# Performance work log

Hardware: AMD Instinct MI355X
Metric: run time of the kernel (lower is better)

The kernel has to match this reference:

```python
import jax, jax.numpy as jnp
import numpy as np

ROT_DIM = 32  # min(32, dim_head)

def rotate_half(t):
    # '... (j d) -> ... j d' with j=2, unbind, cat(-x2, x1)
    x1, x2 = jnp.split(t, 2, axis=-1)
    return jnp.concatenate((-x2, x1), axis=-1)

def apply_rotary(pos, t):
    rot_dim = pos.shape[-1]
    t_rot, t_pass = t[..., :rot_dim], t[..., rot_dim:]
    t_rot = t_rot * jnp.cos(pos) + rotate_half(t_rot) * jnp.sin(pos)
    return jnp.concatenate((t_rot, t_pass), axis=-1)

def setup_inputs() -> dict:
    key = jax.random.key(0)
    k1, k2, k3 = jax.random.split(key, 3)
    b, n, dim = 2, 2048, 2048
    inner = 16 * 128
    x = jax.random.normal(k1, (b, n, dim), dtype=jnp.float32)
    w_qkv = jax.random.normal(k2, (3 * inner, dim), dtype=jnp.float32) * (dim ** -0.5)
    w_out = jax.random.normal(k3, (inner, dim), dtype=jnp.float32) * (inner ** -0.5)
    g = jnp.ones((dim,), dtype=jnp.float32)
    return {"x": x, "w_qkv": w_qkv, "w_out": w_out, "g": g}

def reference(x, w_qkv, w_out, g):
    b, n, dim = x.shape
    h, d = 16, 128
    scale = d ** -0.5
    # NOTE: original code computes qkv from RAW x; the LayerNorm result is unused.
    qkv = jnp.einsum('bnc,fc->bnf', x, w_qkv)  # [b, n, 3*h*d]
    q, k, v = jnp.split(qkv, 3, axis=-1)
    def to_heads(t):  # b n (h d) -> (b h) n d
        return t.reshape(b, n, h, d).transpose(0, 2, 1, 3).reshape(b * h, n, d)
    q, k, v = map(to_heads, (q, k, v))
    # rotary positions: freqs [n, ROT_DIM//2], cat -> [n, ROT_DIM]
    inv_freq = 1.0 / (10000.0 ** (jnp.arange(0, ROT_DIM, 2, dtype=jnp.float32) / ROT_DIM))
    freqs = jnp.arange(n, dtype=jnp.float32)[:, None] * inv_freq[None, :]
    pos = jnp.concatenate((freqs, freqs), axis=-1)  # [n, ROT_DIM]
    q = apply_rotary(pos, q)
    k = apply_rotary(pos, k)
    q = q * scale
    sim = jnp.einsum('bid,bjd->bij', q, k)  # [(b h), n, n]
    causal_mask = jnp.triu(jnp.ones((n, n), dtype=bool), 1)
    neg = -jnp.finfo(sim.dtype).max
    sim = jnp.where(causal_mask[None], neg, sim)
    attn = jax.nn.softmax(sim, axis=-1)
    out = jnp.einsum('bij,bjd->bid', attn, v)  # [(b h), n, d]
    out = out.reshape(b, h, n, d).transpose(0, 2, 1, 3).reshape(b, n, h * d)
    return jnp.einsum('bnf,fc->bnc', out, w_out.T)  # Linear(inner, dim): y = out @ w_out^T with w_out [inner, dim]? see note
```

## Files before the change

### kernel.cpp

```cpp
#include <hip/hip_runtime.h>
#include <hip/hip_bf16.h>
#include <stdint.h>

typedef __bf16 bf16_t;
typedef __bf16 bf16x8 __attribute__((ext_vector_type(8)));
typedef float  f32x4  __attribute__((ext_vector_type(4)));

__device__ __forceinline__ void gload16(const void* gp, void* lp) {
  __builtin_amdgcn_global_load_lds(
      (const __attribute__((address_space(1))) void*)(uintptr_t)gp,
      (__attribute__((address_space(3))) void*)(uintptr_t)lp,
      16, 0, 0);
}

__device__ __forceinline__ f32x4 mfma16(bf16x8 a, bf16x8 b, f32x4 c) {
  return __builtin_amdgcn_mfma_f32_16x16x32_bf16(a, b, c, 0, 0, 0);
}

__device__ __forceinline__ uint32_t pack2(float a, float b) {
  uint16_t ba = __builtin_bit_cast(uint16_t, (bf16_t)a);
  uint16_t bb = __builtin_bit_cast(uint16_t, (bf16_t)b);
  return (uint32_t)ba | ((uint32_t)bb << 16);
}

__global__ __launch_bounds__(256) void cast_f32_to_bf16(const float* __restrict__ in,
                                                        bf16_t* __restrict__ out, int n8) {
  int i = blockIdx.x * 256 + threadIdx.x;
  int stride = gridDim.x * 256;
  for (; i < n8; i += stride) {
    const f32x4* p = (const f32x4*)in + (size_t)i * 2;
    f32x4 a = p[0], b = p[1];
    bf16x8 o;
    o[0] = (bf16_t)a[0]; o[1] = (bf16_t)a[1]; o[2] = (bf16_t)a[2]; o[3] = (bf16_t)a[3];
    o[4] = (bf16_t)b[0]; o[5] = (bf16_t)b[1]; o[6] = (bf16_t)b[2]; o[7] = (bf16_t)b[3];
    ((bf16x8*)out)[i] = o;
  }
}

__global__ __launch_bounds__(512, 2) void gemm_qkv(const bf16_t* __restrict__ A,
                                                   const bf16_t* __restrict__ B,
                                                   bf16_t* __restrict__ C,
                                                   int M, int N, int K) {
  __shared__ __align__(16) bf16_t As[2][256 * 32];
  __shared__ __align__(16) bf16_t Bs[2][384 * 32];
  const int t = threadIdx.x;
  const int wid = t >> 6, l = t & 63;
  const int l15 = l & 15, l4 = l >> 4;
  const int wm = wid >> 2, wn = wid & 3;
  const long m0 = (long)blockIdx.x * 256;
  const long n0 = (long)blockIdx.y * 384;
  const int KT = K >> 5;

  auto stageA = [&](int kt, bf16_t* __restrict__ LB) {
    #pragma unroll
    for (int it = 0; it < 2; ++it) {
      int s = it * 512 + t;
      int r = s >> 2, c = s & 3;
      gload16(A + (m0 + r) * (long)K + kt * 32 + c * 8, LB + r * 32 + c * 8);
    }
  };
  auto stageB = [&](int kt, bf16_t* __restrict__ LB) {
    #pragma unroll
    for (int it = 0; it < 3; ++it) {
      int s = it * 512 + t;
      int r = s >> 2, c = s & 3;
      gload16(B + (n0 + r) * (long)K + kt * 32 + c * 8, LB + r * 32 + c * 8);
    }
  };
  auto ldfrag = [&](const bf16_t* buf, int rloc) -> bf16x8 {
    return *(const bf16x8*)(buf + rloc * 32 + l4 * 8);
  };

  f32x4 acc[8][6] = {};

  stageB(0, &Bs[0][0]);
  stageA(0, &As[0][0]);
  stageB(1, &Bs[1][0]);
  asm volatile("s_waitcnt vmcnt(3)" ::: "memory");
  asm volatile("s_barrier" ::: "memory");

  for (int kt = 0; kt < KT; ++kt) {
    const bf16_t* Ab = &As[kt & 1][0];
    const bf16_t* Bb = &Bs[kt & 1][0];
    const bool stA = (kt + 1 < KT), stB = (kt + 2 < KT);

    bf16x8 bfr[6];
    #pragma unroll
    for (int nr = 0; nr < 6; ++nr) bfr[nr] = ldfrag(Bb, wn * 96 + nr * 16 + l15);
    {
      bf16x8 a0 = ldfrag(Ab, wm * 128 + 0 * 16 + l15);
      bf16x8 a1 = ldfrag(Ab, wm * 128 + 1 * 16 + l15);
      bf16x8 a2 = ldfrag(Ab, wm * 128 + 2 * 16 + l15);
      bf16x8 a3 = ldfrag(Ab, wm * 128 + 3 * 16 + l15);
      if (stA) stageA(kt + 1, &As[(kt + 1) & 1][0]);
      asm volatile("s_barrier" ::: "memory");
      asm volatile("s_waitcnt lgkmcnt(0)" ::: "memory");
      __builtin_amdgcn_sched_barrier(0);
      __builtin_amdgcn_s_setprio(1);
      #pragma unroll
      for (int nr = 0; nr < 6; ++nr) {
        acc[0][nr] = mfma16(a0, bfr[nr], acc[0][nr]);
        acc[1][nr] = mfma16(a1, bfr[nr], acc[1][nr]);
        acc[2][nr] = mfma16(a2, bfr[nr], acc[2][nr]);
        acc[3][nr] = mfma16(a3, bfr[nr], acc[3][nr]);
      }
      __builtin_amdgcn_s_setprio(0);
      asm volatile("s_barrier" ::: "memory");
    }
    {
      bf16x8 a4 = ldfrag(Ab, wm * 128 + 4 * 16 + l15);
      bf16x8 a5 = ldfrag(Ab, wm * 128 + 5 * 16 + l15);
      bf16x8 a6 = ldfrag(Ab, wm * 128 + 6 * 16 + l15);
      bf16x8 a7 = ldfrag(Ab, wm * 128 + 7 * 16 + l15);
      if (stB) stageB(kt + 2, &Bs[kt & 1][0]);
      asm volatile("s_barrier" ::: "memory");
      asm volatile("s_waitcnt lgkmcnt(0)" ::: "memory");
      __builtin_amdgcn_sched_barrier(0);
      __builtin_amdgcn_s_setprio(1);
      #pragma unroll
      for (int nr = 0; nr < 6; ++nr) {
        acc[4][nr] = mfma16(a4, bfr[nr], acc[4][nr]);
        acc[5][nr] = mfma16(a5, bfr[nr], acc[5][nr]);
        acc[6][nr] = mfma16(a6, bfr[nr], acc[6][nr]);
        acc[7][nr] = mfma16(a7, bfr[nr], acc[7][nr]);
      }
      __builtin_amdgcn_s_setprio(0);
      if (stB) asm volatile("s_waitcnt vmcnt(3)" ::: "memory");
      else     asm volatile("s_waitcnt vmcnt(0)" ::: "memory");
      asm volatile("s_barrier" ::: "memory");
    }
  }

  #pragma unroll
  for (int mr = 0; mr < 8; ++mr)
    #pragma unroll
    for (int nr = 0; nr < 6; ++nr)
      #pragma unroll
      for (int i = 0; i < 4; ++i) {
        long r = m0 + wm * 128 + mr * 16 + l4 * 4 + i;
        long c = n0 + wn * 96 + nr * 16 + l15;
        C[r * N + c] = (bf16_t)acc[mr][nr][i];
      }
}

template<bool OUT_BF16>
__global__ __launch_bounds__(512, 2) void gemm8p_bt(const bf16_t* __restrict__ A,
                                                    const bf16_t* __restrict__ B,
                                                    void* __restrict__ Cout,
                                                    int M, int N, int K) {
  __shared__ __align__(16) bf16_t As[2][128 * 64];
  __shared__ __align__(16) bf16_t Bs[2][256 * 64];
  const int t = threadIdx.x;
  const int wid = t >> 6, l = t & 63;
  const int l15 = l & 15, l4 = l >> 4;
  const int wm = wid >> 2, wn = wid & 3;
  const long m0 = (long)blockIdx.x * 128;
  const long n0 = (long)blockIdx.y * 256;
  const int KT = K >> 6;

  auto stageA = [&](int kt, bf16_t* __restrict__ LB) {
    #pragma unroll
    for (int it = 0; it < 2; ++it) {
      int s = it * 512 + t;
      int r = s >> 3, c = s & 7;
      gload16(A + (m0 + r) * (long)K + kt * 64 + ((c ^ (r & 7)) << 3),
              LB + r * 64 + c * 8);
    }
  };
  auto stageB = [&](int kt, bf16_t* __restrict__ LB) {
    #pragma unroll
    for (int it = 0; it < 4; ++it) {
      int s = it * 512 + t;
      int r = s >> 3, c = s & 7;
      gload16(B + (n0 + r) * (long)K + kt * 64 + ((c ^ (r & 7)) << 3),
              LB + r * 64 + c * 8);
    }
  };
  auto ldfrag = [&](const bf16_t* buf, int rloc, int kk) -> bf16x8 {
    return *(const bf16x8*)(buf + rloc * 64 + ((((kk << 2) + l4) ^ (rloc & 7)) << 3));
  };

  f32x4 acc[4][4] = {};

  stageB(0, &Bs[0][0]);
  stageA(0, &As[0][0]);
  stageB(1, &Bs[1][0]);
  asm volatile("s_waitcnt vmcnt(4)" ::: "memory");
  asm volatile("s_barrier" ::: "memory");

  for (int kt = 0; kt < KT; ++kt) {
    const bf16_t* Ab = &As[kt & 1][0];
    const bf16_t* Bb = &Bs[kt & 1][0];
    const bool stA = (kt + 1 < KT), stB = (kt + 2 < KT);

    bf16x8 bfr[4][2];
    #pragma unroll
    for (int nr = 0; nr < 4; ++nr)
      #pragma unroll
      for (int kk = 0; kk < 2; ++kk)
        bfr[nr][kk] = ldfrag(Bb, wn * 64 + nr * 16 + l15, kk);
    {
      bf16x8 a00 = ldfrag(Ab, wm * 64 + 0 * 16 + l15, 0);
      bf16x8 a01 = ldfrag(Ab, wm * 64 + 0 * 16 + l15, 1);
      bf16x8 a10 = ldfrag(Ab, wm * 64 + 1 * 16 + l15, 0);
      bf16x8 a11 = ldfrag(Ab, wm * 64 + 1 * 16 + l15, 1);
      if (stA) stageA(kt + 1, &As[(kt + 1) & 1][0]);
      asm volatile("s_barrier" ::: "memory");
      asm volatile("s_waitcnt lgkmcnt(0)" ::: "memory");
      __builtin_amdgcn_sched_barrier(0);
      __builtin_amdgcn_s_setprio(1);
      #pragma unroll
      for (int nr = 0; nr < 4; ++nr) {
        acc[0][nr] = mfma16(a00, bfr[nr][0], acc[0][nr]);
        acc[0][nr] = mfma16(a01, bfr[nr][1], acc[0][nr]);
        acc[1][nr] = mfma16(a10, bfr[nr][0], acc[1][nr]);
        acc[1][nr] = mfma16(a11, bfr[nr][1], acc[1][nr]);
      }
      __builtin_amdgcn_s_setprio(0);
      asm volatile("s_barrier" ::: "memory");
    }
    {
      bf16x8 a00 = ldfrag(Ab, wm * 64 + 2 * 16 + l15, 0);
      bf16x8 a01 = ldfrag(Ab, wm * 64 + 2 * 16 + l15, 1);
      bf16x8 a10 = ldfrag(Ab, wm * 64 + 3 * 16 + l15, 0);
      bf16x8 a11 = ldfrag(Ab, wm * 64 + 3 * 16 + l15, 1);
      if (stB) stageB(kt + 2, &Bs[kt & 1][0]);
      asm volatile("s_barrier" ::: "memory");
      asm volatile("s_waitcnt lgkmcnt(0)" ::: "memory");
      __builtin_amdgcn_sched_barrier(0);
      __builtin_amdgcn_s_setprio(1);
      #pragma unroll
      for (int nr = 0; nr < 4; ++nr) {
        acc[2][nr] = mfma16(a00, bfr[nr][0], acc[2][nr]);
        acc[2][nr] = mfma16(a01, bfr[nr][1], acc[2][nr]);
        acc[3][nr] = mfma16(a10, bfr[nr][0], acc[3][nr]);
        acc[3][nr] = mfma16(a11, bfr[nr][1], acc[3][nr]);
      }
      __builtin_amdgcn_s_setprio(0);
      if (stB) asm volatile("s_waitcnt vmcnt(4)" ::: "memory");
      else     asm volatile("s_waitcnt vmcnt(0)" ::: "memory");
      asm volatile("s_barrier" ::: "memory");
    }
  }

  #pragma unroll
  for (int mr = 0; mr < 4; ++mr)
    #pragma unroll
    for (int nr = 0; nr < 4; ++nr)
      #pragma unroll
      for (int i = 0; i < 4; ++i) {
        long r = m0 + wm * 64 + mr * 16 + l4 * 4 + i;
        long c = n0 + wn * 64 + nr * 16 + l15;
        if (OUT_BF16) ((bf16_t*)Cout)[r * N + c] = (bf16_t)acc[mr][nr][i];
        else          ((float*)Cout)[r * N + c] = acc[mr][nr][i];
      }
}

__global__ __launch_bounds__(256) void rope_scale(bf16_t* __restrict__ qkv) {
  int t = blockIdx.x * 256 + threadIdx.x;
  int m = t >> 8;
  int h = (t >> 4) & 15;
  int j = t & 15;
  int n = m & 2047;
  const float L2_10000_D16 = 0.8304820237218406f;
  float inv = exp2f(-(float)j * L2_10000_D16);
  float ang = (float)n * inv;
  float s, c;
  sincosf(ang, &s, &c);
  const float scale = 0.08838834764831845f;
  bf16_t* qp = qkv + (long)m * 6144 + h * 128;
  float a = (float)qp[j], b = (float)qp[j + 16];
  qp[j]      = (bf16_t)((a * c - b * s) * scale);
  qp[j + 16] = (bf16_t)((b * c + a * s) * scale);
  #pragma unroll
  for (int u = 0; u < 6; ++u) {
    int d = 32 + j + u * 16;
    qp[d] = (bf16_t)((float)qp[d] * scale);
  }
  bf16_t* kp = qp + 2048;
  a = (float)kp[j]; b = (float)kp[j + 16];
  kp[j]      = (bf16_t)(a * c - b * s);
  kp[j + 16] = (bf16_t)(b * c + a * s);
}

__global__ __launch_bounds__(512, 4) void attn_causal(const bf16_t* __restrict__ qkv,
                                                      bf16_t* __restrict__ ao) {
  const int id = blockIdx.x;
  const int qt = 15 - (id >> 5);
  const int bh = id & 31;
  const int b = bh >> 4, h = bh & 15;
  const int t = threadIdx.x;
  const int wid = t >> 6, l = t & 63;
  const int l15 = l & 15, l4 = l >> 4;
  __shared__ __align__(16) bf16_t Ks0[64 * 128];
  __shared__ __align__(16) bf16_t Ks1[64 * 128];
  __shared__ __align__(16) bf16_t Vt[128 * 64];
  __shared__ __align__(16) bf16_t Pb[8][16 * 72];
  const bf16_t* base = qkv + (long)b * 2048 * 6144 + h * 128;
  const int q0w = qt * 128 + wid * 16;
  bf16x8 qf[4];
  #pragma unroll
  for (int ks = 0; ks < 4; ++ks)
    qf[ks] = *(const bf16x8*)(base + (long)(q0w + l15) * 6144 + ks * 32 + l4 * 8);
  f32x4 o[8] = {};
  float mrun = -1.0e30f, lrun = 0.f;
  bf16_t* pbuf = Pb[wid];
  bf16x8 vr0, vr1;
  const int ntiles = 2 * qt + 2;

  auto stageK = [&](int tile, bf16_t* dst) {
    const bf16_t* src = base + 2048 + (long)tile * 64 * 6144;
    #pragma unroll
    for (int it = 0; it < 2; ++it) {
      int s = it * 512 + t;
      int krow = s >> 4, kc = s & 15;
      int ksc = kc ^ (krow & 7);
      gload16(src + (long)krow * 6144 + ksc * 8, dst + (size_t)s * 8);
    }
  };
  auto loadV = [&](int tile) {
    const bf16_t* vsr = base + 4096 + (long)(tile * 64 + l) * 6144;
    vr0 = *(const bf16x8*)(vsr + wid * 8);
    vr1 = *(const bf16x8*)(vsr + (8 + wid) * 8);
  };
  auto writeVt = [&]() {
    #pragma unroll
    for (int it = 0; it < 2; ++it) {
      int c = it * 8 + wid;
      bf16x8 v = it ? vr1 : vr0;
      #pragma unroll
      for (int e = 0; e < 8; ++e) {
        int d = c * 8 + e;
        Vt[d * 64 + (((l >> 3) ^ e) * 8) + (l & 7)] = v[e];
      }
    }
  };
  auto compute = [&](int kv0, const bf16_t* ksb) {
    if (kv0 > q0w + 15) return;
    f32x4 sa[4] = {};
    __builtin_amdgcn_s_setprio(1);
    #pragma unroll
    for (int ks = 0; ks < 4; ++ks) {
      #pragma unroll
      for (int nb = 0; nb < 4; ++nb) {
        int row = nb * 16 + l15;
        int cs = (ks * 4 + l4) ^ (row & 7);
        bf16x8 kf = *(const bf16x8*)(ksb + row * 128 + cs * 8);
        sa[nb] = mfma16(kf, qf[ks], sa[nb]);
      }
    }
    __builtin_amdgcn_s_setprio(0);
    if (kv0 + 63 > q0w) {
      const int q = q0w + l15;
      #pragma unroll
      for (int nb = 0; nb < 4; ++nb)
        #pragma unroll
        for (int i = 0; i < 4; ++i)
          if (kv0 + nb * 16 + l4 * 4 + i > q) sa[nb][i] = -3.0e38f;
    }
    f32x4 mv;
    #pragma unroll
    for (int i = 0; i < 4; ++i)
      mv[i] = fmaxf(fmaxf(sa[0][i], sa[1][i]), fmaxf(sa[2][i], sa[3][i]));
    float pmax = fmaxf(fmaxf(mv[0], mv[1]), fmaxf(mv[2], mv[3]));
    pmax = fmaxf(pmax, __shfl_xor(pmax, 16));
    pmax = fmaxf(pmax, __shfl_xor(pmax, 32));
    if (!__all(pmax - mrun <= 8.0f)) {
      float mnew = fmaxf(mrun, pmax);
      float corr = __expf(mrun - mnew);
      mrun = mnew;
      lrun *= corr;
      float cc[4];
      #pragma unroll
      for (int i = 0; i < 4; ++i) cc[i] = __shfl(corr, l4 * 4 + i);
      #pragma unroll
      for (int nf = 0; nf < 8; ++nf)
        #pragma unroll
        for (int i = 0; i < 4; ++i) o[nf][i] *= cc[i];
    }
    float ps = 0.f;
    #pragma unroll
    for (int nb = 0; nb < 4; ++nb)
      #pragma unroll
      for (int i = 0; i < 4; ++i) {
        float p = __expf(sa[nb][i] - mrun);
        sa[nb][i] = p;
        ps += p;
      }
    ps += __shfl_xor(ps, 16);
    ps += __shfl_xor(ps, 32);
    lrun += ps;
    #pragma unroll
    for (int nb = 0; nb < 4; ++nb) {
      int cw = (nb * 2 + (l4 >> 1)) ^ (l15 & 7);
      uint32_t* dst = (uint32_t*)(pbuf + l15 * 72 + cw * 8 + (l4 & 1) * 4);
      dst[0] = pack2(sa[nb][0], sa[nb][1]);
      dst[1] = pack2(sa[nb][2], sa[nb][3]);
    }
    #pragma unroll
    for (int ks2 = 0; ks2 < 2; ++ks2) {
      bf16x8 pf = *(const bf16x8*)(pbuf + l15 * 72 + (((ks2 * 4 + l4) ^ (l15 & 7)) * 8));
      __builtin_amdgcn_s_setprio(1);
      #pragma unroll
      for (int nf = 0; nf < 8; ++nf) {
        int row = nf * 16 + l15;
        bf16x8 vf = *(const bf16x8*)(Vt + row * 64 + (((ks2 * 4 + l4) ^ (row & 7)) * 8));
        o[nf] = mfma16(pf, vf, o[nf]);
      }
      __builtin_amdgcn_s_setprio(0);
    }
  };

  stageK(0, Ks0);
  loadV(0);
  writeVt();
  __syncthreads();
  for (int tile = 0; tile < ntiles; ++tile) {
    bf16_t* cur = (tile & 1) ? Ks1 : Ks0;
    bf16_t* nxt = (tile & 1) ? Ks0 : Ks1;
    const bool pre = (tile + 1 < ntiles);
    if (pre) { stageK(tile + 1, nxt); loadV(tile + 1); }
    compute(tile * 64, cur);
    __syncthreads();
    if (pre) writeVt();
    __syncthreads();
  }
  float linv = 1.f / lrun;
  float li[4];
  #pragma unroll
  for (int i = 0; i < 4; ++i) li[i] = __shfl(linv, l4 * 4 + i);
  bf16_t* aob = ao + (long)b * 2048 * 2048 + h * 128;
  #pragma unroll
  for (int i = 0; i < 4; ++i) {
    long qrow = q0w + l4 * 4 + i;
    #pragma unroll
    for (int nf = 0; nf < 8; ++nf)
      aob[qrow * 2048 + nf * 16 + l15] = (bf16_t)(o[nf][i] * li[i]);
  }
}

extern "C" void kernel_launch(void* const* d_in, const int* in_sizes, int n_in,
                              void* d_out, int out_size, void* d_ws, size_t ws_size,
                              hipStream_t stream) {
  const float* x     = (const float*)d_in[0];
  const float* w_qkv = (const float*)d_in[1];
  const float* w_out = (const float*)d_in[2];
  char* ws = (char*)d_ws;
  bf16_t* xb    = (bf16_t*)(ws + 0L);
  bf16_t* wqkvb = (bf16_t*)(ws + 16777216L);
  bf16_t* woutb = (bf16_t*)(ws + 41943040L);
  bf16_t* qkv   = (bf16_t*)(ws + 50331648L);
  bf16_t* ao    = (bf16_t*)(ws + 100663296L);

  cast_f32_to_bf16<<<2048, 256, 0, stream>>>(x, xb, 1048576);
  cast_f32_to_bf16<<<2048, 256, 0, stream>>>(w_qkv, wqkvb, 1572864);
  cast_f32_to_bf16<<<1024, 256, 0, stream>>>(w_out, woutb, 524288);
  gemm_qkv<<<dim3(16, 16), 512, 0, stream>>>(xb, wqkvb, qkv, 4096, 6144, 2048);
  rope_scale<<<4096, 256, 0, stream>>>(qkv);
  attn_causal<<<512, 512, 0, stream>>>(qkv, ao);
  gemm8p_bt<false><<<dim3(32, 8), 512, 0, stream>>>(ao, woutb, d_out, 4096, 2048, 2048);
}
```

Baseline: 256.3 us.

## Fuse RoPE and q-scale into QKV GEMM epilogue, swizzle LDS, rebalance attention tiles

The standalone rope_scale kernel is removed. Rotary embedding and the query scaling are now applied in the epilogue of the QKV GEMM, while the fp32 accumulators are still in registers. The GEMM's LDS tiles gain an XOR swizzle on the 16-byte chunk index to reduce bank conflicts on fragment loads. The attention block-to-query-tile mapping now interleaves heavy and light causal tiles, so the second half of the grid runs light tiles first. The cost is more register pressure and sincos work in the GEMM epilogue, in exchange for one fewer kernel launch and one fewer read-modify-write pass over q and k in global memory.

```diff
diff --git a/kernel.cpp b/kernel.cpp
--- a/kernel.cpp
+++ b/kernel.cpp
@@ -56,7 +56,8 @@
     for (int it = 0; it < 2; ++it) {
       int s = it * 512 + t;
       int r = s >> 2, c = s & 3;
-      gload16(A + (m0 + r) * (long)K + kt * 32 + c * 8, LB + r * 32 + c * 8);
+      int cs = c ^ ((r >> 1) & 3);
+      gload16(A + (m0 + r) * (long)K + kt * 32 + cs * 8, LB + r * 32 + c * 8);
     }
   };
   auto stageB = [&](int kt, bf16_t* __restrict__ LB) {
@@ -64,11 +65,13 @@
     for (int it = 0; it < 3; ++it) {
       int s = it * 512 + t;
       int r = s >> 2, c = s & 3;
-      gload16(B + (n0 + r) * (long)K + kt * 32 + c * 8, LB + r * 32 + c * 8);
+      int cs = c ^ ((r >> 1) & 3);
+      gload16(B + (n0 + r) * (long)K + kt * 32 + cs * 8, LB + r * 32 + c * 8);
     }
   };
   auto ldfrag = [&](const bf16_t* buf, int rloc) -> bf16x8 {
-    return *(const bf16x8*)(buf + rloc * 32 + l4 * 8);
+    int cs = l4 ^ ((rloc >> 1) & 3);
+    return *(const bf16x8*)(buf + rloc * 32 + cs * 8);
   };
 
   f32x4 acc[8][6] = {};
@@ -131,16 +134,42 @@
     }
   }
 
+  const int nrA = ((128 - ((wn * 96) & 127)) & 127) >> 4;
+  const float L2D16 = 0.8304820237218406f;
+  const float invf = exp2f(-(float)l15 * L2D16);
+  const float qscale = 0.08838834764831845f;
   #pragma unroll
-  for (int mr = 0; mr < 8; ++mr)
-    #pragma unroll
-    for (int nr = 0; nr < 6; ++nr)
-      #pragma unroll
-      for (int i = 0; i < 4; ++i) {
-        long r = m0 + wm * 128 + mr * 16 + l4 * 4 + i;
-        long c = n0 + wn * 96 + nr * 16 + l15;
-        C[r * N + c] = (bf16_t)acc[mr][nr][i];
-      }
+  for (int mr = 0; mr < 8; ++mr) {
+    const long r0 = m0 + wm * 128 + mr * 16 + l4 * 4;
+    if (nrA < 6) {
+      const long fA = n0 + wn * 96 + nrA * 16;
+      if (fA < 4096) {
+        float sv[4], cv[4];
+        #pragma unroll
+        for (int i = 0; i < 4; ++i) {
+          float ang = (float)((int)(r0 + i) & 2047) * invf;
+          sincosf(ang, &sv[i], &cv[i]);
+        }
+        #pragma unroll
+        for (int i = 0; i < 4; ++i) {
+          float a = acc[mr][nrA][i], b2 = acc[mr][nrA + 1][i];
+          acc[mr][nrA][i]     = a * cv[i] - b2 * sv[i];
+          acc[mr][nrA + 1][i] = b2 * cv[i] + a * sv[i];
+        }
+      }
+    }
+    #pragma unroll
+    for (int nr = 0; nr < 6; ++nr) {
+      const long f0 = n0 + wn * 96 + nr * 16;
+      if (f0 < 2048) {
+        #pragma unroll
+        for (int i = 0; i < 4; ++i) acc[mr][nr][i] *= qscale;
+      }
+      #pragma unroll
+      for (int i = 0; i < 4; ++i)
+        C[(r0 + i) * N + f0 + l15] = (bf16_t)acc[mr][nr][i];
+    }
+  }
 }
 
 template<bool OUT_BF16>
@@ -256,37 +285,10 @@
       }
 }
 
-__global__ __launch_bounds__(256) void rope_scale(bf16_t* __restrict__ qkv) {
-  int t = blockIdx.x * 256 + threadIdx.x;
-  int m = t >> 8;
-  int h = (t >> 4) & 15;
-  int j = t & 15;
-  int n = m & 2047;
-  const float L2_10000_D16 = 0.8304820237218406f;
-  float inv = exp2f(-(float)j * L2_10000_D16);
-  float ang = (float)n * inv;
-  float s, c;
-  sincosf(ang, &s, &c);
-  const float scale = 0.08838834764831845f;
-  bf16_t* qp = qkv + (long)m * 6144 + h * 128;
-  float a = (float)qp[j], b = (float)qp[j + 16];
-  qp[j]      = (bf16_t)((a * c - b * s) * scale);
-  qp[j + 16] = (bf16_t)((b * c + a * s) * scale);
-  #pragma unroll
-  for (int u = 0; u < 6; ++u) {
-    int d = 32 + j + u * 16;
-    qp[d] = (bf16_t)((float)qp[d] * scale);
-  }
-  bf16_t* kp = qp + 2048;
-  a = (float)kp[j]; b = (float)kp[j + 16];
-  kp[j]      = (bf16_t)(a * c - b * s);
-  kp[j + 16] = (bf16_t)(b * c + a * s);
-}
-
 __global__ __launch_bounds__(512, 4) void attn_causal(const bf16_t* __restrict__ qkv,
                                                       bf16_t* __restrict__ ao) {
   const int id = blockIdx.x;
-  const int qt = 15 - (id >> 5);
+  const int qt = (id < 256) ? (15 - (id >> 5)) : ((id - 256) >> 5);
   const int bh = id & 31;
   const int b = bh >> 4, h = bh & 15;
   const int t = threadIdx.x;
@@ -456,7 +458,6 @@
   cast_f32_to_bf16<<<2048, 256, 0, stream>>>(w_qkv, wqkvb, 1572864);
   cast_f32_to_bf16<<<1024, 256, 0, stream>>>(w_out, woutb, 524288);
   gemm_qkv<<<dim3(16, 16), 512, 0, stream>>>(xb, wqkvb, qkv, 4096, 6144, 2048);
-  rope_scale<<<4096, 256, 0, stream>>>(qkv);
   attn_causal<<<512, 512, 0, stream>>>(qkv, ao);
   gemm8p_bt<false><<<dim3(32, 8), 512, 0, stream>>>(ao, woutb, d_out, 4096, 2048, 2048);
 }
```

Result: slower. 303.7 us (+18.5%).
